# Optimization experiments

Hardware: AMD Instinct MI355X
Metric: run time of the kernel (lower is better)

The kernel has to match this reference:

```python
import jax, jax.numpy as jnp
import numpy as np

N, M, E, C_IN, C_OUT = 100000, 20000, 1600000, 128, 128


def _safe_inv(d):
    # 1/d with 0 where d==0 (matches PyG D[D==inf]=0), grad-safe
    safe = jnp.where(d > 0, d, 1.0)
    return jnp.where(d > 0, 1.0 / safe, 0.0)


def _hconv(x, node_idx, edge_idx, hw, W, b):
    # PyG HypergraphConv, use_attention=False, heads=1:
    # X' = D^{-1} H B^{-1} H^T (X Theta) + bias, D uses hyperedge_weight
    xt = x @ W  # [N, C_OUT]
    D = jax.ops.segment_sum(hw[edge_idx], node_idx, num_segments=N)
    Dinv = _safe_inv(D)  # [N]
    Bc = jax.ops.segment_sum(jnp.ones((E,), dtype=x.dtype), edge_idx, num_segments=M)
    Binv = _safe_inv(Bc)  # [M]
    # node -> hyperedge (message weighted by B^{-1} of target edge)
    e = jax.ops.segment_sum(Binv[edge_idx][:, None] * xt[node_idx], edge_idx, num_segments=M)
    # hyperedge -> node (message weighted by D^{-1} of target node)
    out = jax.ops.segment_sum(Dinv[node_idx][:, None] * e[edge_idx], node_idx, num_segments=N)
    return out + b


def setup_inputs() -> dict:
    key = jax.random.key(0)
    ks = jax.random.split(key, 12)
    x = jax.random.normal(ks[0], (N, C_IN), dtype=jnp.float32)
    node_idx = jax.random.randint(ks[1], (E,), 0, N, dtype=jnp.int32)
    edge_idx = jax.random.randint(ks[2], (E,), 0, M, dtype=jnp.int32)
    hyperedge_index = jnp.stack([node_idx, edge_idx])
    hyperedge_weight = jax.random.uniform(ks[3], (M,), dtype=jnp.float32) + 0.5
    hyperedge_attr = jax.random.normal(ks[4], (M, C_IN), dtype=jnp.float32)
    batch = jnp.zeros((N,), dtype=jnp.int32)
    s1 = 1.0 / np.sqrt(C_IN)
    s2 = 1.0 / np.sqrt(C_OUT)
    W1 = jax.random.uniform(ks[5], (C_IN, C_OUT), minval=-s1, maxval=s1, dtype=jnp.float32)
    W2 = jax.random.uniform(ks[6], (C_OUT, C_OUT), minval=-s2, maxval=s2, dtype=jnp.float32)
    W3 = jax.random.uniform(ks[7], (C_OUT, C_OUT), minval=-s2, maxval=s2, dtype=jnp.float32)
    b1 = jax.random.uniform(ks[8], (C_OUT,), minval=-s1, maxval=s1, dtype=jnp.float32)
    b2 = jax.random.uniform(ks[9], (C_OUT,), minval=-s2, maxval=s2, dtype=jnp.float32)
    b3 = jax.random.uniform(ks[10], (C_OUT,), minval=-s2, maxval=s2, dtype=jnp.float32)
    return {"x": x, "hyperedge_index": hyperedge_index, "hyperedge_weight": hyperedge_weight,
            "hyperedge_attr": hyperedge_attr, "batch": batch,
            "W1": W1, "b1": b1, "W2": W2, "b2": b2, "W3": W3, "b3": b3}


def reference(x, hyperedge_index, hyperedge_weight, hyperedge_attr, batch,
              W1, b1, W2, b2, W3, b3):
    node_idx = hyperedge_index[0]
    edge_idx = hyperedge_index[1]
    # dropout is identity in eval mode; hyperedge_attr/batch unused (no attention)
    h = jax.nn.relu(_hconv(x, node_idx, edge_idx, hyperedge_weight, W1, b1))
    h = jax.nn.relu(_hconv(h, node_idx, edge_idx, hyperedge_weight, W2, b2))
    h = jax.nn.relu(_hconv(h, node_idx, edge_idx, hyperedge_weight, W3, b3))
    return h
```

## Files before the change

### kernel.cpp

```cpp
#include <hip/hip_runtime.h>
#include <hip/hip_fp16.h>

#define NN 100000
#define MM 20000
#define EE 1600000

#define NBLK_E 256
#define CHUNK_E (EE / NBLK_E)
#define NBLK_N 128
#define CHUNK_N (EE / NBLK_N)
#define NRANGE2 50000
#define FN_PASSES 8
#define FN_RANGE (NN / FN_PASSES)

#define SCAN_BLOCK 256
#define SCAN_ITEMS 8
#define SCAN_TILE (SCAN_BLOCK * SCAN_ITEMS)
#define NB_E ((MM + SCAN_TILE - 1) / SCAN_TILE)
#define NB_N ((NN + SCAN_TILE - 1) / SCAN_TILE)
#define NB_TOT (NB_E + NB_N)

static inline size_t align256(size_t x) { return (x + 255) & ~(size_t)255; }

struct alignas(8) half4 { __half2 lo, hi; };

__device__ __forceinline__ float4 h4_to_f4(half4 v) {
  float2 a = __half22float2(v.lo);
  float2 b = __half22float2(v.hi);
  return make_float4(a.x, a.y, b.x, b.y);
}
__device__ __forceinline__ half4 f4_to_h4(float4 v) {
  half4 r;
  r.lo = __float22half2_rn(make_float2(v.x, v.y));
  r.hi = __float22half2_rn(make_float2(v.z, v.w));
  return r;
}

__global__ __launch_bounds__(256) void cvt_f2h_kernel(
    const float* __restrict__ in, __half* __restrict__ out, int n4) {
  int i = blockIdx.x * 256 + threadIdx.x;
  int stride = gridDim.x * 256;
  for (; i < n4; i += stride) {
    float4 v = ((const float4*)in)[i];
    ((half4*)out)[i] = f4_to_h4(v);
  }
}

__global__ __launch_bounds__(256) void ehist_kernel(
    const int* __restrict__ edge_idx,
    unsigned short* __restrict__ bcnt_e, unsigned short* __restrict__ lrank_e) {
  extern __shared__ int hist[];
  int b = blockIdx.x;
  for (int k = threadIdx.x; k < MM; k += 256) hist[k] = 0;
  __syncthreads();
  int lo = b * CHUNK_E, hi = lo + CHUNK_E;
  for (int i = lo + threadIdx.x; i < hi; i += 256) {
    int e = edge_idx[i];
    int r = atomicAdd(&hist[e], 1);
    lrank_e[i] = (unsigned short)r;
  }
  __syncthreads();
  unsigned short* row = bcnt_e + (size_t)b * MM;
  for (int k = threadIdx.x; k < MM / 2; k += 256) {
    ushort2 w;
    w.x = (unsigned short)hist[2 * k];
    w.y = (unsigned short)hist[2 * k + 1];
    ((ushort2*)row)[k] = w;
  }
}

__global__ __launch_bounds__(256) void nhist_kernel(
    const int* __restrict__ node_idx,
    unsigned short* __restrict__ bcnt_n, unsigned short* __restrict__ lrank_n) {
  extern __shared__ unsigned int histp[];
  int b = blockIdx.x;
  int lo = b * CHUNK_N, hi = lo + CHUNK_N;
  unsigned short* row = bcnt_n + (size_t)b * NN;
  for (int p = 0; p < 2; ++p) {
    int base = p * NRANGE2;
    for (int k = threadIdx.x; k < NRANGE2 / 2; k += 256) histp[k] = 0;
    __syncthreads();
    for (int i = lo + threadIdx.x; i < hi; i += 256) {
      int n = node_idx[i] - base;
      if ((unsigned)n < (unsigned)NRANGE2) {
        unsigned add = (n & 1) ? 0x10000u : 1u;
        unsigned old = atomicAdd(&histp[n >> 1], add);
        lrank_n[i] = (unsigned short)((old >> ((n & 1) * 16)) & 0xFFFFu);
      }
    }
    __syncthreads();
    for (int k = threadIdx.x; k < NRANGE2 / 2; k += 256) {
      unsigned w = histp[k];
      ushort2 o;
      o.x = (unsigned short)(w & 0xFFFFu);
      o.y = (unsigned short)(w >> 16);
      ((ushort2*)(row + base))[k] = o;
    }
    __syncthreads();
  }
}

__global__ __launch_bounds__(256) void colscan_kernel(
    unsigned short* __restrict__ bcnt_e, unsigned short* __restrict__ bcnt_n,
    int* __restrict__ ecnt, int* __restrict__ ncnt) {
  int i = blockIdx.x * 256 + threadIdx.x;
  if (i < MM) {
    int run = 0;
#pragma unroll 8
    for (int b = 0; b < NBLK_E; ++b) {
      size_t idx = (size_t)b * MM + i;
      int v = bcnt_e[idx];
      bcnt_e[idx] = (unsigned short)run;
      run += v;
    }
    ecnt[i] = run;
  } else if (i < MM + NN) {
    int n = i - MM;
    int run = 0;
#pragma unroll 8
    for (int b = 0; b < NBLK_N; ++b) {
      size_t idx = (size_t)b * NN + n;
      int v = bcnt_n[idx];
      bcnt_n[idx] = (unsigned short)run;
      run += v;
    }
    ncnt[n] = run;
  }
}

__global__ __launch_bounds__(SCAN_BLOCK) void scan_partial_kernel(
    const int* __restrict__ ecnt, const int* __restrict__ ncnt,
    int* __restrict__ eptr, int* __restrict__ nptr, int* __restrict__ bsum) {
  __shared__ int lds[SCAN_BLOCK];
  int b = blockIdx.x;
  const int* cnt; int* ptr; int len; int lb;
  if (b < NB_E) { cnt = ecnt; ptr = eptr; len = MM; lb = b; }
  else          { cnt = ncnt; ptr = nptr; len = NN; lb = b - NB_E; }
  int t = threadIdx.x;
  int lo = lb * SCAN_TILE + t * SCAN_ITEMS;
  int v[SCAN_ITEMS];
  int s = 0;
#pragma unroll
  for (int j = 0; j < SCAN_ITEMS; ++j) {
    int idx = lo + j;
    v[j] = (idx < len) ? cnt[idx] : 0;
    s += v[j];
  }
  lds[t] = s;
  __syncthreads();
  for (int d = 1; d < SCAN_BLOCK; d <<= 1) {
    int o = (t >= d) ? lds[t - d] : 0;
    __syncthreads();
    lds[t] += o;
    __syncthreads();
  }
  int run = lds[t] - s;
#pragma unroll
  for (int j = 0; j < SCAN_ITEMS; ++j) {
    int idx = lo + j;
    if (idx < len) ptr[idx] = run;
    run += v[j];
  }
  if (t == SCAN_BLOCK - 1) bsum[b] = lds[t];
}

__global__ void scan_bsum_kernel(int* __restrict__ bsum) {
  int t = threadIdx.x;
  if (t == 0) {
    int run = 0;
    for (int i = 0; i < NB_E; ++i) { int c = bsum[i]; bsum[i] = run; run += c; }
  } else if (t == 1) {
    int run = 0;
    for (int i = NB_E; i < NB_TOT; ++i) { int c = bsum[i]; bsum[i] = run; run += c; }
  }
}

__global__ __launch_bounds__(SCAN_BLOCK) void scan_fixup_kernel(
    int* __restrict__ eptr, int* __restrict__ nptr,
    const int* __restrict__ ecnt, const int* __restrict__ bsum,
    float* __restrict__ Binv) {
  int b = blockIdx.x;
  int* ptr; int len; int lb; bool isE;
  if (b < NB_E) { ptr = eptr; len = MM; lb = b; isE = true; }
  else          { ptr = nptr; len = NN; lb = b - NB_E; isE = false; }
  int boff = bsum[b];
  int t = threadIdx.x;
  int lo = lb * SCAN_TILE + t * SCAN_ITEMS;
#pragma unroll
  for (int j = 0; j < SCAN_ITEMS; ++j) {
    int idx = lo + j;
    if (idx < len) {
      ptr[idx] += boff;
      if (isE) {
        int c = ecnt[idx];
        Binv[idx] = (c > 0) ? 1.0f / (float)c : 0.0f;
      }
    }
  }
  if (b == 0 && t == 0) { eptr[MM] = EE; nptr[NN] = EE; }
}

__global__ __launch_bounds__(256) void fill_edge_kernel(
    const int* __restrict__ node_idx, const int* __restrict__ edge_idx,
    const int* __restrict__ eptr,
    const unsigned short* __restrict__ bcnt_e,
    const unsigned short* __restrict__ lrank_e,
    int* __restrict__ edge_nodes) {
  __shared__ unsigned short rowb[MM];
  int b = blockIdx.x;
  const unsigned short* src = bcnt_e + (size_t)b * MM;
  for (int k = threadIdx.x; k < MM / 2; k += 256)
    ((ushort2*)rowb)[k] = ((const ushort2*)src)[k];
  __syncthreads();
  int lo = b * CHUNK_E, hi = lo + CHUNK_E;
  for (int i = lo + threadIdx.x; i < hi; i += 256) {
    int e = edge_idx[i];
    int slot = eptr[e] + (int)rowb[e] + (int)lrank_e[i];
    edge_nodes[slot] = node_idx[i];
  }
}

__global__ __launch_bounds__(256) void fill_node_kernel(
    const int* __restrict__ node_idx, const int* __restrict__ edge_idx,
    const int* __restrict__ nptr,
    const unsigned short* __restrict__ bcnt_n,
    const unsigned short* __restrict__ lrank_n,
    int* __restrict__ node_edges) {
  __shared__ unsigned short rowslice[FN_RANGE];
  int p = blockIdx.x / NBLK_N;
  int b = blockIdx.x % NBLK_N;
  int base = p * FN_RANGE;
  const unsigned short* row = bcnt_n + (size_t)b * NN + base;
  for (int k = threadIdx.x; k < FN_RANGE / 2; k += 256)
    ((ushort2*)rowslice)[k] = ((const ushort2*)row)[k];
  __syncthreads();
  int lo = b * CHUNK_N, hi = lo + CHUNK_N;
  for (int i = lo + threadIdx.x; i < hi; i += 256) {
    int n = node_idx[i] - base;
    if ((unsigned)n < (unsigned)FN_RANGE) {
      int slot = nptr[n + base] + (int)rowslice[n] + (int)lrank_n[i];
      node_edges[slot] = edge_idx[i];
    }
  }
}

__global__ __launch_bounds__(256) void dinv_csr_kernel(
    const int* __restrict__ nptr, const int* __restrict__ node_edges,
    const float* __restrict__ hw, float* __restrict__ Dinv) {
  int n = blockIdx.x * 256 + threadIdx.x;
  if (n >= NN) return;
  int lo = nptr[n], hi = nptr[n + 1];
  float d = 0.0f;
  for (int j = lo; j < hi; ++j) d += hw[node_edges[j]];
  Dinv[n] = (d > 0.0f) ? 1.0f / d : 0.0f;
}

__device__ __forceinline__ void fma4(float4& acc, float s, const float4& m) {
  acc.x += s * m.x;
  acc.y += s * m.y;
  acc.z += s * m.z;
  acc.w += s * m.w;
}

__global__ __launch_bounds__(256) void gemm128_kernel(
    const __half* __restrict__ X, const float* __restrict__ W,
    __half* __restrict__ Y, int nrows) {
  __shared__ float Wl[128 * 128];
  float4* Wl4 = (float4*)Wl;
  const float4* W4 = (const float4*)W;
  for (int i = threadIdx.x; i < 128 * 32; i += 256) Wl4[i] = W4[i];
  __syncthreads();

  int tc = threadIdx.x & 15;
  int tr = threadIdx.x >> 4;
  int base = blockIdx.x * 64;
  int r[4];
  bool v[4];
#pragma unroll
  for (int j = 0; j < 4; ++j) {
    int rr = base + tr + j * 16;
    v[j] = rr < nrows;
    r[j] = v[j] ? rr : 0;
  }
  float4 acc[4][2];
#pragma unroll
  for (int j = 0; j < 4; ++j) {
    acc[j][0] = make_float4(0.f, 0.f, 0.f, 0.f);
    acc[j][1] = make_float4(0.f, 0.f, 0.f, 0.f);
  }
#pragma unroll 4
  for (int k4 = 0; k4 < 32; ++k4) {
    float4 xv[4];
#pragma unroll
    for (int j = 0; j < 4; ++j)
      xv[j] = h4_to_f4(((const half4*)X)[(size_t)r[j] * 32 + k4]);
#pragma unroll
    for (int kk = 0; kk < 4; ++kk) {
      float4 wva = Wl4[(k4 * 4 + kk) * 32 + tc];
      float4 wvb = Wl4[(k4 * 4 + kk) * 32 + 16 + tc];
#pragma unroll
      for (int j = 0; j < 4; ++j) {
        float xk = ((const float*)&xv[j])[kk];
        fma4(acc[j][0], xk, wva);
        fma4(acc[j][1], xk, wvb);
      }
    }
  }
#pragma unroll
  for (int j = 0; j < 4; ++j) {
    if (v[j]) {
      ((half4*)Y)[(size_t)r[j] * 32 + tc] = f4_to_h4(acc[j][0]);
      ((half4*)Y)[(size_t)r[j] * 32 + 16 + tc] = f4_to_h4(acc[j][1]);
    }
  }
}

__global__ __launch_bounds__(256) void edge_agg_kernel(
    const __half* __restrict__ hin, const int* __restrict__ eptr,
    const int* __restrict__ edge_nodes, const float* __restrict__ Binv,
    __half* __restrict__ eout) {
  int half_id = threadIdx.x >> 5;
  int lane = threadIdx.x & 31;
  int m = blockIdx.x * 8 + half_id;
  if (m >= MM) return;
  int lo = eptr[m], hi = eptr[m + 1];
  const half4* h4p = (const half4*)hin;
  float4 acc = make_float4(0.f, 0.f, 0.f, 0.f);
  int j = lo;
  for (; j + 8 <= hi; j += 8) {
    int idx[8];
#pragma unroll
    for (int u = 0; u < 8; ++u) idx[u] = edge_nodes[j + u];
    float4 s[8];
#pragma unroll
    for (int u = 0; u < 8; ++u) s[u] = h4_to_f4(h4p[(size_t)idx[u] * 32 + lane]);
    acc.x += ((s[0].x + s[1].x) + (s[2].x + s[3].x)) + ((s[4].x + s[5].x) + (s[6].x + s[7].x));
    acc.y += ((s[0].y + s[1].y) + (s[2].y + s[3].y)) + ((s[4].y + s[5].y) + (s[6].y + s[7].y));
    acc.z += ((s[0].z + s[1].z) + (s[2].z + s[3].z)) + ((s[4].z + s[5].z) + (s[6].z + s[7].z));
    acc.w += ((s[0].w + s[1].w) + (s[2].w + s[3].w)) + ((s[4].w + s[5].w) + (s[6].w + s[7].w));
  }
  for (; j < hi; ++j) {
    int n = edge_nodes[j];
    float4 a = h4_to_f4(h4p[(size_t)n * 32 + lane]);
    acc.x += a.x; acc.y += a.y; acc.z += a.z; acc.w += a.w;
  }
  float bi = Binv[m];
  acc.x *= bi; acc.y *= bi; acc.z *= bi; acc.w *= bi;
  ((half4*)eout)[(size_t)m * 32 + lane] = f4_to_h4(acc);
}

__device__ __forceinline__ void strow_q(float* Y, size_t row, int q, float4 v) {
  ((float4*)Y)[row * 32 + q] = v;
}
__device__ __forceinline__ void strow_q(__half* Y, size_t row, int q, float4 v) {
  ((half4*)Y)[row * 32 + q] = f4_to_h4(v);
}

template <typename TOUT>
__global__ __launch_bounds__(256) void node_agg_half_kernel(
    const __half* __restrict__ ein, const int* __restrict__ nptr,
    const int* __restrict__ node_edges, const float* __restrict__ Dinv,
    const float* __restrict__ bias, TOUT* __restrict__ out) {
  int nb = NN / 16;
  int c4 = (blockIdx.x >= nb) ? 16 : 0;
  int eb = (blockIdx.x >= nb) ? blockIdx.x - nb : blockIdx.x;
  int g = threadIdx.x >> 4;
  int gl = threadIdx.x & 15;
  int n = eb * 16 + g;
  int q = c4 + gl;
  int lo = nptr[n], hi = nptr[n + 1];
  const half4* e4 = (const half4*)ein;
  float4 acc = make_float4(0.f, 0.f, 0.f, 0.f);
  int j = lo;
  for (; j + 4 <= hi; j += 4) {
    int m0 = node_edges[j + 0];
    int m1 = node_edges[j + 1];
    int m2 = node_edges[j + 2];
    int m3 = node_edges[j + 3];
    float4 a = h4_to_f4(e4[(size_t)m0 * 32 + q]);
    float4 b = h4_to_f4(e4[(size_t)m1 * 32 + q]);
    float4 c = h4_to_f4(e4[(size_t)m2 * 32 + q]);
    float4 d = h4_to_f4(e4[(size_t)m3 * 32 + q]);
    acc.x += (a.x + b.x) + (c.x + d.x);
    acc.y += (a.y + b.y) + (c.y + d.y);
    acc.z += (a.z + b.z) + (c.z + d.z);
    acc.w += (a.w + b.w) + (c.w + d.w);
  }
  for (; j < hi; ++j) {
    int m = node_edges[j];
    float4 a = h4_to_f4(e4[(size_t)m * 32 + q]);
    acc.x += a.x; acc.y += a.y; acc.z += a.z; acc.w += a.w;
  }
  float di = Dinv[n];
  float4 bb = ((const float4*)bias)[q];
  float4 rv;
  rv.x = fmaxf(di * acc.x + bb.x, 0.f);
  rv.y = fmaxf(di * acc.y + bb.y, 0.f);
  rv.z = fmaxf(di * acc.z + bb.z, 0.f);
  rv.w = fmaxf(di * acc.w + bb.w, 0.f);
  strow_q(out, (size_t)n, q, rv);
}

extern "C" void kernel_launch(void* const* d_in, const int* in_sizes, int n_in,
                              void* d_out, int out_size, void* d_ws, size_t ws_size,
                              hipStream_t stream) {
  const float* x = (const float*)d_in[0];
  const int* hidx = (const int*)d_in[1];
  const int* node_idx = hidx;
  const int* edge_idx = hidx + EE;
  const float* hw = (const float*)d_in[2];
  const float* W1 = (const float*)d_in[5];
  const float* b1 = (const float*)d_in[6];
  const float* W2 = (const float*)d_in[7];
  const float* b2 = (const float*)d_in[8];
  const float* W3 = (const float*)d_in[9];
  const float* b3 = (const float*)d_in[10];
  float* out = (float*)d_out;

  char* ws = (char*)d_ws;
  size_t off = 0;
  auto alloc = [&](size_t bytes) -> char* {
    char* p = ws + off;
    off = align256(off + bytes);
    return p;
  };
  __half* xh   = (__half*)alloc(sizeof(__half) * (size_t)NN * 128);
  __half* h    = (__half*)alloc(sizeof(__half) * (size_t)NN * 128);
  __half* eraw = (__half*)alloc(sizeof(__half) * (size_t)MM * 128);
  __half* et   = (__half*)alloc(sizeof(__half) * (size_t)MM * 128);
  unsigned short* bcnt_e = (unsigned short*)alloc(sizeof(short) * (size_t)NBLK_E * MM);
  unsigned short* bcnt_n = (unsigned short*)alloc(sizeof(short) * (size_t)NBLK_N * NN);
  unsigned short* lrank_e = (unsigned short*)alloc(sizeof(short) * (size_t)EE);
  unsigned short* lrank_n = (unsigned short*)alloc(sizeof(short) * (size_t)EE);
  int*   ecnt  = (int*)alloc(sizeof(int) * MM);
  int*   ncnt  = (int*)alloc(sizeof(int) * NN);
  int*   eptr  = (int*)alloc(sizeof(int) * (MM + 1));
  int*   nptr  = (int*)alloc(sizeof(int) * (NN + 1));
  int*   bsum  = (int*)alloc(sizeof(int) * NB_TOT);
  float* Binv  = (float*)alloc(sizeof(float) * MM);
  float* Dinv  = (float*)alloc(sizeof(float) * NN);
  int* edge_nodes = (int*)alloc(sizeof(int) * (size_t)EE);
  int* node_edges = (int*)alloc(sizeof(int) * (size_t)EE);
  (void)ws_size; (void)in_sizes; (void)n_in; (void)out_size;

  ehist_kernel<<<NBLK_E, 256, MM * sizeof(int), stream>>>(edge_idx, bcnt_e, lrank_e);
  nhist_kernel<<<NBLK_N, 256, (NRANGE2 / 2) * sizeof(int), stream>>>(node_idx, bcnt_n, lrank_n);
  colscan_kernel<<<(MM + NN + 255) / 256, 256, 0, stream>>>(bcnt_e, bcnt_n, ecnt, ncnt);
  scan_partial_kernel<<<NB_TOT, SCAN_BLOCK, 0, stream>>>(ecnt, ncnt, eptr, nptr, bsum);
  scan_bsum_kernel<<<1, 64, 0, stream>>>(bsum);
  scan_fixup_kernel<<<NB_TOT, SCAN_BLOCK, 0, stream>>>(eptr, nptr, ecnt, bsum, Binv);
  fill_edge_kernel<<<NBLK_E, 256, 0, stream>>>(node_idx, edge_idx, eptr,
                                               bcnt_e, lrank_e, edge_nodes);
  fill_node_kernel<<<FN_PASSES * NBLK_N, 256, 0, stream>>>(
      node_idx, edge_idx, nptr, bcnt_n, lrank_n, node_edges);
  dinv_csr_kernel<<<(NN + 255) / 256, 256, 0, stream>>>(nptr, node_edges, hw, Dinv);
  cvt_f2h_kernel<<<1024, 256, 0, stream>>>(x, xh, NN * 32);

  const int gemmE_grid = (MM + 63) / 64;
  const int eagg_grid = MM / 8;
  const int nagg_grid = 2 * (NN / 16);

  edge_agg_kernel<<<eagg_grid, 256, 0, stream>>>(xh, eptr, edge_nodes, Binv, eraw);
  gemm128_kernel<<<gemmE_grid, 256, 0, stream>>>(eraw, W1, et, MM);
  node_agg_half_kernel<__half><<<nagg_grid, 256, 0, stream>>>(et, nptr, node_edges, Dinv, b1, h);
  edge_agg_kernel<<<eagg_grid, 256, 0, stream>>>(h, eptr, edge_nodes, Binv, eraw);
  gemm128_kernel<<<gemmE_grid, 256, 0, stream>>>(eraw, W2, et, MM);
  node_agg_half_kernel<__half><<<nagg_grid, 256, 0, stream>>>(et, nptr, node_edges, Dinv, b2, xh);
  edge_agg_kernel<<<eagg_grid, 256, 0, stream>>>(xh, eptr, edge_nodes, Binv, eraw);
  gemm128_kernel<<<gemmE_grid, 256, 0, stream>>>(eraw, W3, et, MM);
  node_agg_half_kernel<float><<<nagg_grid, 256, 0, stream>>>(et, nptr, node_edges, Dinv, b3, out);
}
```

Before: 578.4 us.

## Store node features in column panels and split edge gather by panel

Node feature buffers in half precision are now kept in a panel layout: eight column panels of 16 channels, each holding all nodes contiguously. The edge aggregation kernel gives each block one panel, so every gathered row is a 32-byte piece read by 4 lanes, with 8 neighbours in flight per edge, then reduces across lanes with shuffles. The aim is to shrink the working set each block touches so gathers hit L2 better, and to raise memory-level parallelism. The cost is that each neighbour index is read once per panel, eight times in total, plus an extra shuffle reduction. The node aggregation writes and the initial conversion are adapted to the new layout.

```diff
diff --git a/kernel.cpp b/kernel.cpp
--- a/kernel.cpp
+++ b/kernel.cpp
@@ -4,6 +4,10 @@
 #define NN 100000
 #define MM 20000
 #define EE 1600000
+
+#define NPANEL 8
+#define EPB 8
+#define EGRP (MM / EPB)
 
 #define NBLK_E 256
 #define CHUNK_E (EE / NBLK_E)
@@ -36,13 +40,21 @@
   return r;
 }
 
-__global__ __launch_bounds__(256) void cvt_f2h_kernel(
-    const float* __restrict__ in, __half* __restrict__ out, int n4) {
+__device__ __forceinline__ void st_node(__half* Y, size_t n, int q, float4 v) {
+  ((half4*)Y)[(((size_t)(q >> 2)) * NN + n) * 4 + (q & 3)] = f4_to_h4(v);
+}
+__device__ __forceinline__ void st_node(float* Y, size_t n, int q, float4 v) {
+  ((float4*)Y)[n * 32 + q] = v;
+}
+
+__global__ __launch_bounds__(256) void cvt_f2h_panel_kernel(
+    const float* __restrict__ in, __half* __restrict__ out) {
   int i = blockIdx.x * 256 + threadIdx.x;
   int stride = gridDim.x * 256;
-  for (; i < n4; i += stride) {
+  for (; i < NN * 32; i += stride) {
+    int n = i >> 5, q = i & 31;
     float4 v = ((const float4*)in)[i];
-    ((half4*)out)[i] = f4_to_h4(v);
+    st_node(out, (size_t)n, q, v);
   }
 }
 
@@ -315,45 +327,36 @@
   }
 }
 
-__global__ __launch_bounds__(256) void edge_agg_kernel(
-    const __half* __restrict__ hin, const int* __restrict__ eptr,
-    const int* __restrict__ edge_nodes, const float* __restrict__ Binv,
-    __half* __restrict__ eout) {
+__global__ __launch_bounds__(256) void edge_agg_panel_kernel(
+    const __half* __restrict__ hp,
+    const int* __restrict__ eptr, const int* __restrict__ edge_nodes,
+    const float* __restrict__ Binv, __half* __restrict__ eout) {
+  int p = blockIdx.x & 7;
+  int eb = blockIdx.x >> 3;
   int half_id = threadIdx.x >> 5;
-  int lane = threadIdx.x & 31;
-  int m = blockIdx.x * 8 + half_id;
-  if (m >= MM) return;
+  int l = threadIdx.x & 31;
+  int m = eb * EPB + half_id;
   int lo = eptr[m], hi = eptr[m + 1];
-  const half4* h4p = (const half4*)hin;
+  int piece = l & 3;
+  const half4* base = (const half4*)hp + (size_t)p * NN * 4;
   float4 acc = make_float4(0.f, 0.f, 0.f, 0.f);
-  int j = lo;
-  for (; j + 8 <= hi; j += 8) {
-    int idx[8];
-#pragma unroll
-    for (int u = 0; u < 8; ++u) idx[u] = edge_nodes[j + u];
-    float4 s[8];
-#pragma unroll
-    for (int u = 0; u < 8; ++u) s[u] = h4_to_f4(h4p[(size_t)idx[u] * 32 + lane]);
-    acc.x += ((s[0].x + s[1].x) + (s[2].x + s[3].x)) + ((s[4].x + s[5].x) + (s[6].x + s[7].x));
-    acc.y += ((s[0].y + s[1].y) + (s[2].y + s[3].y)) + ((s[4].y + s[5].y) + (s[6].y + s[7].y));
-    acc.z += ((s[0].z + s[1].z) + (s[2].z + s[3].z)) + ((s[4].z + s[5].z) + (s[6].z + s[7].z));
-    acc.w += ((s[0].w + s[1].w) + (s[2].w + s[3].w)) + ((s[4].w + s[5].w) + (s[6].w + s[7].w));
-  }
-  for (; j < hi; ++j) {
+  for (int j = lo + (l >> 2); j < hi; j += 8) {
     int n = edge_nodes[j];
-    float4 a = h4_to_f4(h4p[(size_t)n * 32 + lane]);
+    float4 a = h4_to_f4(base[(size_t)n * 4 + piece]);
     acc.x += a.x; acc.y += a.y; acc.z += a.z; acc.w += a.w;
   }
-  float bi = Binv[m];
-  acc.x *= bi; acc.y *= bi; acc.z *= bi; acc.w *= bi;
-  ((half4*)eout)[(size_t)m * 32 + lane] = f4_to_h4(acc);
-}
-
-__device__ __forceinline__ void strow_q(float* Y, size_t row, int q, float4 v) {
-  ((float4*)Y)[row * 32 + q] = v;
-}
-__device__ __forceinline__ void strow_q(__half* Y, size_t row, int q, float4 v) {
-  ((half4*)Y)[row * 32 + q] = f4_to_h4(v);
+#pragma unroll
+  for (int mask = 4; mask <= 16; mask <<= 1) {
+    acc.x += __shfl_xor(acc.x, mask, 64);
+    acc.y += __shfl_xor(acc.y, mask, 64);
+    acc.z += __shfl_xor(acc.z, mask, 64);
+    acc.w += __shfl_xor(acc.w, mask, 64);
+  }
+  if ((l >> 2) == 0) {
+    float bi = Binv[m];
+    acc.x *= bi; acc.y *= bi; acc.z *= bi; acc.w *= bi;
+    ((half4*)eout)[(size_t)m * 32 + p * 4 + piece] = f4_to_h4(acc);
+  }
 }
 
 template <typename TOUT>
@@ -398,7 +401,7 @@
   rv.y = fmaxf(di * acc.y + bb.y, 0.f);
   rv.z = fmaxf(di * acc.z + bb.z, 0.f);
   rv.w = fmaxf(di * acc.w + bb.w, 0.f);
-  strow_q(out, (size_t)n, q, rv);
+  st_node(out, (size_t)n, q, rv);
 }
 
 extern "C" void kernel_launch(void* const* d_in, const int* in_sizes, int n_in,
@@ -454,19 +457,19 @@
   fill_node_kernel<<<FN_PASSES * NBLK_N, 256, 0, stream>>>(
       node_idx, edge_idx, nptr, bcnt_n, lrank_n, node_edges);
   dinv_csr_kernel<<<(NN + 255) / 256, 256, 0, stream>>>(nptr, node_edges, hw, Dinv);
-  cvt_f2h_kernel<<<1024, 256, 0, stream>>>(x, xh, NN * 32);
+  cvt_f2h_panel_kernel<<<1024, 256, 0, stream>>>(x, xh);
 
   const int gemmE_grid = (MM + 63) / 64;
-  const int eagg_grid = MM / 8;
+  const int eagg_grid = NPANEL * EGRP;
   const int nagg_grid = 2 * (NN / 16);
 
-  edge_agg_kernel<<<eagg_grid, 256, 0, stream>>>(xh, eptr, edge_nodes, Binv, eraw);
+  edge_agg_panel_kernel<<<eagg_grid, 256, 0, stream>>>(xh, eptr, edge_nodes, Binv, eraw);
   gemm128_kernel<<<gemmE_grid, 256, 0, stream>>>(eraw, W1, et, MM);
   node_agg_half_kernel<__half><<<nagg_grid, 256, 0, stream>>>(et, nptr, node_edges, Dinv, b1, h);
-  edge_agg_kernel<<<eagg_grid, 256, 0, stream>>>(h, eptr, edge_nodes, Binv, eraw);
+  edge_agg_panel_kernel<<<eagg_grid, 256, 0, stream>>>(h, eptr, edge_nodes, Binv, eraw);
   gemm128_kernel<<<gemmE_grid, 256, 0, stream>>>(eraw, W2, et, MM);
   node_agg_half_kernel<__half><<<nagg_grid, 256, 0, stream>>>(et, nptr, node_edges, Dinv, b2, xh);
-  edge_agg_kernel<<<eagg_grid, 256, 0, stream>>>(xh, eptr, edge_nodes, Binv, eraw);
+  edge_agg_panel_kernel<<<eagg_grid, 256, 0, stream>>>(xh, eptr, edge_nodes, Binv, eraw);
   gemm128_kernel<<<gemmE_grid, 256, 0, stream>>>(eraw, W3, et, MM);
   node_agg_half_kernel<float><<<nagg_grid, 256, 0, stream>>>(et, nptr, node_edges, Dinv, b3, out);
 }
```

New measurement: 646.4 us. 1.12x slower.

## Merge preprocessing kernels and use one 32-lane group per node in aggregation

Applied to the files above, without the earlier changes.

Independent preprocessing kernels are merged into single launches with block-index dispatch: edge and node histograms, edge and node CSR fills, and the Dinv computation plus the input conversion to fp16. The node aggregation now gives each node a full 32-lane group covering all 128 channels, where before 16 lanes covered half the channels across two grid halves. This removes launch gaps and lets independent work share the GPU, and it halves the per-node index reads in aggregation. In exchange, blocks of different shared-memory needs share one kernel, so the histogram kernel reserves the larger shared allocation for every block, which may lower occupancy.

```diff
diff --git a/kernel.cpp b/kernel.cpp
--- a/kernel.cpp
+++ b/kernel.cpp
@@ -12,6 +12,9 @@
 #define NRANGE2 50000
 #define FN_PASSES 8
 #define FN_RANGE (NN / FN_PASSES)
+#define FILL_NODE_BLOCKS (FN_PASSES * NBLK_N)
+#define DINV_BLOCKS ((NN + 255) / 256)
+#define CVT_BLOCKS 1024
 
 #define SCAN_BLOCK 256
 #define SCAN_ITEMS 8
@@ -36,67 +39,57 @@
   return r;
 }
 
-__global__ __launch_bounds__(256) void cvt_f2h_kernel(
-    const float* __restrict__ in, __half* __restrict__ out, int n4) {
-  int i = blockIdx.x * 256 + threadIdx.x;
-  int stride = gridDim.x * 256;
-  for (; i < n4; i += stride) {
-    float4 v = ((const float4*)in)[i];
-    ((half4*)out)[i] = f4_to_h4(v);
-  }
-}
-
-__global__ __launch_bounds__(256) void ehist_kernel(
-    const int* __restrict__ edge_idx,
-    unsigned short* __restrict__ bcnt_e, unsigned short* __restrict__ lrank_e) {
-  extern __shared__ int hist[];
-  int b = blockIdx.x;
-  for (int k = threadIdx.x; k < MM; k += 256) hist[k] = 0;
-  __syncthreads();
-  int lo = b * CHUNK_E, hi = lo + CHUNK_E;
-  for (int i = lo + threadIdx.x; i < hi; i += 256) {
-    int e = edge_idx[i];
-    int r = atomicAdd(&hist[e], 1);
-    lrank_e[i] = (unsigned short)r;
-  }
-  __syncthreads();
-  unsigned short* row = bcnt_e + (size_t)b * MM;
-  for (int k = threadIdx.x; k < MM / 2; k += 256) {
-    ushort2 w;
-    w.x = (unsigned short)hist[2 * k];
-    w.y = (unsigned short)hist[2 * k + 1];
-    ((ushort2*)row)[k] = w;
-  }
-}
-
-__global__ __launch_bounds__(256) void nhist_kernel(
-    const int* __restrict__ node_idx,
+__global__ __launch_bounds__(256) void hist_kernel(
+    const int* __restrict__ node_idx, const int* __restrict__ edge_idx,
+    unsigned short* __restrict__ bcnt_e, unsigned short* __restrict__ lrank_e,
     unsigned short* __restrict__ bcnt_n, unsigned short* __restrict__ lrank_n) {
-  extern __shared__ unsigned int histp[];
-  int b = blockIdx.x;
-  int lo = b * CHUNK_N, hi = lo + CHUNK_N;
-  unsigned short* row = bcnt_n + (size_t)b * NN;
-  for (int p = 0; p < 2; ++p) {
-    int base = p * NRANGE2;
-    for (int k = threadIdx.x; k < NRANGE2 / 2; k += 256) histp[k] = 0;
-    __syncthreads();
+  extern __shared__ int smem[];
+  if (blockIdx.x < NBLK_E) {
+    int* hist = smem;
+    int b = blockIdx.x;
+    for (int k = threadIdx.x; k < MM; k += 256) hist[k] = 0;
+    __syncthreads();
+    int lo = b * CHUNK_E, hi = lo + CHUNK_E;
     for (int i = lo + threadIdx.x; i < hi; i += 256) {
-      int n = node_idx[i] - base;
-      if ((unsigned)n < (unsigned)NRANGE2) {
-        unsigned add = (n & 1) ? 0x10000u : 1u;
-        unsigned old = atomicAdd(&histp[n >> 1], add);
-        lrank_n[i] = (unsigned short)((old >> ((n & 1) * 16)) & 0xFFFFu);
+      int e = edge_idx[i];
+      int r = atomicAdd(&hist[e], 1);
+      lrank_e[i] = (unsigned short)r;
+    }
+    __syncthreads();
+    unsigned short* row = bcnt_e + (size_t)b * MM;
+    for (int k = threadIdx.x; k < MM / 2; k += 256) {
+      ushort2 w;
+      w.x = (unsigned short)hist[2 * k];
+      w.y = (unsigned short)hist[2 * k + 1];
+      ((ushort2*)row)[k] = w;
+    }
+  } else {
+    unsigned int* histp = (unsigned int*)smem;
+    int b = blockIdx.x - NBLK_E;
+    int lo = b * CHUNK_N, hi = lo + CHUNK_N;
+    unsigned short* row = bcnt_n + (size_t)b * NN;
+    for (int p = 0; p < 2; ++p) {
+      int base = p * NRANGE2;
+      for (int k = threadIdx.x; k < NRANGE2 / 2; k += 256) histp[k] = 0;
+      __syncthreads();
+      for (int i = lo + threadIdx.x; i < hi; i += 256) {
+        int n = node_idx[i] - base;
+        if ((unsigned)n < (unsigned)NRANGE2) {
+          unsigned add = (n & 1) ? 0x10000u : 1u;
+          unsigned old = atomicAdd(&histp[n >> 1], add);
+          lrank_n[i] = (unsigned short)((old >> ((n & 1) * 16)) & 0xFFFFu);
+        }
       }
-    }
-    __syncthreads();
-    for (int k = threadIdx.x; k < NRANGE2 / 2; k += 256) {
-      unsigned w = histp[k];
-      ushort2 o;
-      o.x = (unsigned short)(w & 0xFFFFu);
-      o.y = (unsigned short)(w >> 16);
-      ((ushort2*)(row + base))[k] = o;
-    }
-    __syncthreads();
+      __syncthreads();
+      for (int k = threadIdx.x; k < NRANGE2 / 2; k += 256) {
+        unsigned w = histp[k];
+        ushort2 o;
+        o.x = (unsigned short)(w & 0xFFFFu);
+        o.y = (unsigned short)(w >> 16);
+        ((ushort2*)(row + base))[k] = o;
+      }
+      __syncthreads();
+    }
   }
 }
 
@@ -200,59 +193,66 @@
   if (b == 0 && t == 0) { eptr[MM] = EE; nptr[NN] = EE; }
 }
 
-__global__ __launch_bounds__(256) void fill_edge_kernel(
+__global__ __launch_bounds__(256) void fill_kernel(
     const int* __restrict__ node_idx, const int* __restrict__ edge_idx,
-    const int* __restrict__ eptr,
+    const int* __restrict__ eptr, const int* __restrict__ nptr,
     const unsigned short* __restrict__ bcnt_e,
+    const unsigned short* __restrict__ bcnt_n,
     const unsigned short* __restrict__ lrank_e,
-    int* __restrict__ edge_nodes) {
-  __shared__ unsigned short rowb[MM];
-  int b = blockIdx.x;
-  const unsigned short* src = bcnt_e + (size_t)b * MM;
-  for (int k = threadIdx.x; k < MM / 2; k += 256)
-    ((ushort2*)rowb)[k] = ((const ushort2*)src)[k];
-  __syncthreads();
-  int lo = b * CHUNK_E, hi = lo + CHUNK_E;
-  for (int i = lo + threadIdx.x; i < hi; i += 256) {
-    int e = edge_idx[i];
-    int slot = eptr[e] + (int)rowb[e] + (int)lrank_e[i];
-    edge_nodes[slot] = node_idx[i];
-  }
-}
-
-__global__ __launch_bounds__(256) void fill_node_kernel(
-    const int* __restrict__ node_idx, const int* __restrict__ edge_idx,
-    const int* __restrict__ nptr,
-    const unsigned short* __restrict__ bcnt_n,
     const unsigned short* __restrict__ lrank_n,
-    int* __restrict__ node_edges) {
-  __shared__ unsigned short rowslice[FN_RANGE];
-  int p = blockIdx.x / NBLK_N;
-  int b = blockIdx.x % NBLK_N;
-  int base = p * FN_RANGE;
-  const unsigned short* row = bcnt_n + (size_t)b * NN + base;
-  for (int k = threadIdx.x; k < FN_RANGE / 2; k += 256)
-    ((ushort2*)rowslice)[k] = ((const ushort2*)row)[k];
-  __syncthreads();
-  int lo = b * CHUNK_N, hi = lo + CHUNK_N;
-  for (int i = lo + threadIdx.x; i < hi; i += 256) {
-    int n = node_idx[i] - base;
-    if ((unsigned)n < (unsigned)FN_RANGE) {
-      int slot = nptr[n + base] + (int)rowslice[n] + (int)lrank_n[i];
-      node_edges[slot] = edge_idx[i];
-    }
-  }
-}
-
-__global__ __launch_bounds__(256) void dinv_csr_kernel(
+    int* __restrict__ edge_nodes, int* __restrict__ node_edges) {
+  extern __shared__ unsigned short srow[];
+  if (blockIdx.x < NBLK_E) {
+    int b = blockIdx.x;
+    const unsigned short* src = bcnt_e + (size_t)b * MM;
+    for (int k = threadIdx.x; k < MM / 2; k += 256)
+      ((ushort2*)srow)[k] = ((const ushort2*)src)[k];
+    __syncthreads();
+    int lo = b * CHUNK_E, hi = lo + CHUNK_E;
+    for (int i = lo + threadIdx.x; i < hi; i += 256) {
+      int e = edge_idx[i];
+      int slot = eptr[e] + (int)srow[e] + (int)lrank_e[i];
+      edge_nodes[slot] = node_idx[i];
+    }
+  } else {
+    int bid = blockIdx.x - NBLK_E;
+    int p = bid / NBLK_N;
+    int b = bid % NBLK_N;
+    int base = p * FN_RANGE;
+    const unsigned short* row = bcnt_n + (size_t)b * NN + base;
+    for (int k = threadIdx.x; k < FN_RANGE / 2; k += 256)
+      ((ushort2*)srow)[k] = ((const ushort2*)row)[k];
+    __syncthreads();
+    int lo = b * CHUNK_N, hi = lo + CHUNK_N;
+    for (int i = lo + threadIdx.x; i < hi; i += 256) {
+      int n = node_idx[i] - base;
+      if ((unsigned)n < (unsigned)FN_RANGE) {
+        int slot = nptr[n + base] + (int)srow[n] + (int)lrank_n[i];
+        node_edges[slot] = edge_idx[i];
+      }
+    }
+  }
+}
+
+__global__ __launch_bounds__(256) void dinv_cvt_kernel(
     const int* __restrict__ nptr, const int* __restrict__ node_edges,
-    const float* __restrict__ hw, float* __restrict__ Dinv) {
-  int n = blockIdx.x * 256 + threadIdx.x;
-  if (n >= NN) return;
-  int lo = nptr[n], hi = nptr[n + 1];
-  float d = 0.0f;
-  for (int j = lo; j < hi; ++j) d += hw[node_edges[j]];
-  Dinv[n] = (d > 0.0f) ? 1.0f / d : 0.0f;
+    const float* __restrict__ hw, float* __restrict__ Dinv,
+    const float* __restrict__ x, __half* __restrict__ xh) {
+  if (blockIdx.x < DINV_BLOCKS) {
+    int n = blockIdx.x * 256 + threadIdx.x;
+    if (n >= NN) return;
+    int lo = nptr[n], hi = nptr[n + 1];
+    float d = 0.0f;
+    for (int j = lo; j < hi; ++j) d += hw[node_edges[j]];
+    Dinv[n] = (d > 0.0f) ? 1.0f / d : 0.0f;
+  } else {
+    int i = (blockIdx.x - DINV_BLOCKS) * 256 + threadIdx.x;
+    int stride = CVT_BLOCKS * 256;
+    for (; i < NN * 32; i += stride) {
+      float4 v = ((const float4*)x)[i];
+      ((half4*)xh)[i] = f4_to_h4(v);
+    }
+  }
 }
 
 __device__ __forceinline__ void fma4(float4& acc, float s, const float4& m) {
@@ -349,25 +349,22 @@
   ((half4*)eout)[(size_t)m * 32 + lane] = f4_to_h4(acc);
 }
 
-__device__ __forceinline__ void strow_q(float* Y, size_t row, int q, float4 v) {
-  ((float4*)Y)[row * 32 + q] = v;
-}
-__device__ __forceinline__ void strow_q(__half* Y, size_t row, int q, float4 v) {
-  ((half4*)Y)[row * 32 + q] = f4_to_h4(v);
+__device__ __forceinline__ void strow(float* Y, size_t i, float4 v) {
+  ((float4*)Y)[i] = v;
+}
+__device__ __forceinline__ void strow(__half* Y, size_t i, float4 v) {
+  ((half4*)Y)[i] = f4_to_h4(v);
 }
 
 template <typename TOUT>
-__global__ __launch_bounds__(256) void node_agg_half_kernel(
+__global__ __launch_bounds__(256) void node_agg_kernel(
     const __half* __restrict__ ein, const int* __restrict__ nptr,
     const int* __restrict__ node_edges, const float* __restrict__ Dinv,
     const float* __restrict__ bias, TOUT* __restrict__ out) {
-  int nb = NN / 16;
-  int c4 = (blockIdx.x >= nb) ? 16 : 0;
-  int eb = (blockIdx.x >= nb) ? blockIdx.x - nb : blockIdx.x;
-  int g = threadIdx.x >> 4;
-  int gl = threadIdx.x & 15;
-  int n = eb * 16 + g;
-  int q = c4 + gl;
+  int half_id = threadIdx.x >> 5;
+  int lane = threadIdx.x & 31;
+  int n = blockIdx.x * 8 + half_id;
+  if (n >= NN) return;
   int lo = nptr[n], hi = nptr[n + 1];
   const half4* e4 = (const half4*)ein;
   float4 acc = make_float4(0.f, 0.f, 0.f, 0.f);
@@ -377,10 +374,10 @@
     int m1 = node_edges[j + 1];
     int m2 = node_edges[j + 2];
     int m3 = node_edges[j + 3];
-    float4 a = h4_to_f4(e4[(size_t)m0 * 32 + q]);
-    float4 b = h4_to_f4(e4[(size_t)m1 * 32 + q]);
-    float4 c = h4_to_f4(e4[(size_t)m2 * 32 + q]);
-    float4 d = h4_to_f4(e4[(size_t)m3 * 32 + q]);
+    float4 a = h4_to_f4(e4[(size_t)m0 * 32 + lane]);
+    float4 b = h4_to_f4(e4[(size_t)m1 * 32 + lane]);
+    float4 c = h4_to_f4(e4[(size_t)m2 * 32 + lane]);
+    float4 d = h4_to_f4(e4[(size_t)m3 * 32 + lane]);
     acc.x += (a.x + b.x) + (c.x + d.x);
     acc.y += (a.y + b.y) + (c.y + d.y);
     acc.z += (a.z + b.z) + (c.z + d.z);
@@ -388,17 +385,17 @@
   }
   for (; j < hi; ++j) {
     int m = node_edges[j];
-    float4 a = h4_to_f4(e4[(size_t)m * 32 + q]);
+    float4 a = h4_to_f4(e4[(size_t)m * 32 + lane]);
     acc.x += a.x; acc.y += a.y; acc.z += a.z; acc.w += a.w;
   }
   float di = Dinv[n];
-  float4 bb = ((const float4*)bias)[q];
+  float4 bb = ((const float4*)bias)[lane];
   float4 rv;
   rv.x = fmaxf(di * acc.x + bb.x, 0.f);
   rv.y = fmaxf(di * acc.y + bb.y, 0.f);
   rv.z = fmaxf(di * acc.z + bb.z, 0.f);
   rv.w = fmaxf(di * acc.w + bb.w, 0.f);
-  strow_q(out, (size_t)n, q, rv);
+  strow(out, (size_t)n * 32 + lane, rv);
 }
 
 extern "C" void kernel_launch(void* const* d_in, const int* in_sizes, int n_in,
@@ -443,30 +440,29 @@
   int* node_edges = (int*)alloc(sizeof(int) * (size_t)EE);
   (void)ws_size; (void)in_sizes; (void)n_in; (void)out_size;
 
-  ehist_kernel<<<NBLK_E, 256, MM * sizeof(int), stream>>>(edge_idx, bcnt_e, lrank_e);
-  nhist_kernel<<<NBLK_N, 256, (NRANGE2 / 2) * sizeof(int), stream>>>(node_idx, bcnt_n, lrank_n);
+  hist_kernel<<<NBLK_E + NBLK_N, 256, (NRANGE2 / 2) * sizeof(int), stream>>>(
+      node_idx, edge_idx, bcnt_e, lrank_e, bcnt_n, lrank_n);
   colscan_kernel<<<(MM + NN + 255) / 256, 256, 0, stream>>>(bcnt_e, bcnt_n, ecnt, ncnt);
   scan_partial_kernel<<<NB_TOT, SCAN_BLOCK, 0, stream>>>(ecnt, ncnt, eptr, nptr, bsum);
   scan_bsum_kernel<<<1, 64, 0, stream>>>(bsum);
   scan_fixup_kernel<<<NB_TOT, SCAN_BLOCK, 0, stream>>>(eptr, nptr, ecnt, bsum, Binv);
-  fill_edge_kernel<<<NBLK_E, 256, 0, stream>>>(node_idx, edge_idx, eptr,
-                                               bcnt_e, lrank_e, edge_nodes);
-  fill_node_kernel<<<FN_PASSES * NBLK_N, 256, 0, stream>>>(
-      node_idx, edge_idx, nptr, bcnt_n, lrank_n, node_edges);
-  dinv_csr_kernel<<<(NN + 255) / 256, 256, 0, stream>>>(nptr, node_edges, hw, Dinv);
-  cvt_f2h_kernel<<<1024, 256, 0, stream>>>(x, xh, NN * 32);
+  fill_kernel<<<NBLK_E + FILL_NODE_BLOCKS, 256, MM * sizeof(short), stream>>>(
+      node_idx, edge_idx, eptr, nptr, bcnt_e, bcnt_n, lrank_e, lrank_n,
+      edge_nodes, node_edges);
+  dinv_cvt_kernel<<<DINV_BLOCKS + CVT_BLOCKS, 256, 0, stream>>>(
+      nptr, node_edges, hw, Dinv, x, xh);
 
   const int gemmE_grid = (MM + 63) / 64;
   const int eagg_grid = MM / 8;
-  const int nagg_grid = 2 * (NN / 16);
+  const int nagg_grid = NN / 8;
 
   edge_agg_kernel<<<eagg_grid, 256, 0, stream>>>(xh, eptr, edge_nodes, Binv, eraw);
   gemm128_kernel<<<gemmE_grid, 256, 0, stream>>>(eraw, W1, et, MM);
-  node_agg_half_kernel<__half><<<nagg_grid, 256, 0, stream>>>(et, nptr, node_edges, Dinv, b1, h);
+  node_agg_kernel<__half><<<nagg_grid, 256, 0, stream>>>(et, nptr, node_edges, Dinv, b1, h);
   edge_agg_kernel<<<eagg_grid, 256, 0, stream>>>(h, eptr, edge_nodes, Binv, eraw);
   gemm128_kernel<<<gemmE_grid, 256, 0, stream>>>(eraw, W2, et, MM);
-  node_agg_half_kernel<__half><<<nagg_grid, 256, 0, stream>>>(et, nptr, node_edges, Dinv, b2, xh);
+  node_agg_kernel<__half><<<nagg_grid, 256, 0, stream>>>(et, nptr, node_edges, Dinv, b2, xh);
   edge_agg_kernel<<<eagg_grid, 256, 0, stream>>>(xh, eptr, edge_nodes, Binv, eraw);
   gemm128_kernel<<<gemmE_grid, 256, 0, stream>>>(eraw, W3, et, MM);
-  node_agg_half_kernel<float><<<nagg_grid, 256, 0, stream>>>(et, nptr, node_edges, Dinv, b3, out);
-}
+  node_agg_kernel<float><<<nagg_grid, 256, 0, stream>>>(et, nptr, node_edges, Dinv, b3, out);
+}
```

After: 564.9 us. -2.3%, faster.
